# Optimization experiments

Measured on AMD Instinct MI355X. Metric: run time of the kernel, lower is better.

## Reference

```python
import jax, jax.numpy as jnp
import numpy as np

W_SIZE = 16
WIN = 2 * W_SIZE + 1
OUT_F = 256
MODEL = 512  # output_features * 2


def setup_inputs() -> dict:
    key = jax.random.key(0)
    ks = jax.random.split(key, 7)
    B, T = 4, 2048
    s = 0.02
    return {
        "x": jax.random.normal(ks[0], (B, T, MODEL), jnp.float32),
        "encoder_outputs": jax.random.normal(ks[1], (B, T, OUT_F), jnp.float32),
        # Attention: attn Linear (OUT_F + MODEL -> OUT_F), v Linear (OUT_F -> 1, no bias)
        "W_attn": jax.random.normal(ks[2], (OUT_F + MODEL, OUT_F), jnp.float32) * s,
        "b_attn": jnp.zeros((OUT_F,), jnp.float32),
        "v": jax.random.normal(ks[3], (OUT_F,), jnp.float32) * s,
        # final linear: (MODEL + OUT_F -> OUT_F)
        "W_lin": jax.random.normal(ks[4], (MODEL + OUT_F, OUT_F), jnp.float32) * s,
        "b_lin": jnp.zeros((OUT_F,), jnp.float32),
    }


def _windows(enc):
    B, T, F = enc.shape
    padded = jnp.pad(enc, ((0, 0), (W_SIZE, W_SIZE), (0, 0)))
    idx = jnp.arange(T)[:, None] + jnp.arange(WIN)[None, :]
    return padded[:, idx]


def reference(x, encoder_outputs, W_attn, b_attn, v, W_lin, b_lin):
    win = _windows(encoder_outputs)
    B, T, W, F = win.shape
    # additive (Bahdanau) score: concat(hidden, window) -> Linear -> tanh -> v
    Wh, We = W_attn[:MODEL], W_attn[MODEL:]
    energy = jnp.tanh(
        jnp.einsum('btm,mo->bto', x, Wh)[:, :, None, :]
        + jnp.einsum('btwf,fo->btwo', win, We)
        + b_attn
    )
    scores = jnp.einsum('btwo,o->btw', energy, v)
    a = jax.nn.softmax(scores, axis=-1)
    weighted = jnp.einsum('btw,btwf->btf', a, win)        # [B, T, F]
    h = jnp.concatenate([x, weighted], axis=-1)           # [B, T, MODEL+F]
    out = jax.nn.sigmoid(jnp.einsum('btk,ko->bto', h, W_lin) + b_lin)
    return out, a[:, :, None, :]
```

## Files before the change

### kernel.cpp

```cpp
#include <hip/hip_runtime.h>
#include <math.h>

#define T_DIM 2048
#define B_DIM 4
#define BT (B_DIM * T_DIM)
#define MODEL 512
#define OUTF 256
#define WSZ 16
#define WIN 33

#define BM 128
#define BN 64
#define BK 32

#define TB 16
#define HALO 48
#define TS 72

#define ESCALE 2.885390081777927f
#define ECLAMP 30.0f

typedef __attribute__((ext_vector_type(8))) short bf16x8;
typedef __attribute__((ext_vector_type(4))) float f32x4;

__device__ inline unsigned short f2bf(float f) {
  unsigned int u = __float_as_uint(f);
  u += 0x7fffu + ((u >> 16) & 1u);
  return (unsigned short)(u >> 16);
}
__device__ inline float bflo(unsigned int u) {
  return __uint_as_float(u << 16);
}
__device__ inline float bfhi(unsigned int u) {
  return __uint_as_float(u & 0xffff0000u);
}
__device__ inline float fast_sigmoid(float z) {
  return __builtin_amdgcn_rcpf(1.f + __expf(-z));
}

template <int KS, int MODE>
__device__ __forceinline__ void gemm_body(
    unsigned short (*As)[BM * 40], unsigned short (*Bs)[BN * 40], int rb,
    const float* __restrict__ A, int lda,
    const float* __restrict__ W_attn, const float* __restrict__ W_lin,
    const float* __restrict__ b_attn, const float* __restrict__ b_lin,
    unsigned short* __restrict__ outb, float* __restrict__ outf,
    unsigned short* __restrict__ outb2) {
  const int tid = threadIdx.x;
  const int cb = rb >> 6, rp = rb & 63;
  const int row0 = rp * BM;
  const int colg = (cb & 3) * 64;
  const float* Wsrc = (cb < 4) ? W_attn : W_lin;
  constexpr int wrow0 = (MODE == 0) ? 0 : 512;

  const int arow = tid >> 2, akp = (tid & 3) * 8;
  const int brow = tid >> 4, bcp = (tid & 15) * 4;
  const int bkey = (bcp >> 3) & 3;
  const float* aptr = A + (size_t)(row0 + arow) * lda + akp;
  const float* bptr = Wsrc + (size_t)(wrow0 + brow) * OUTF + colg + bcp;

  float4 ra0[2], ra1[2], rbw[2];
  auto LOADS = [&](int sl, int ks) {
    const float* ap = aptr + ks * BK;
    ra0[sl] = *(const float4*)ap;
    ra1[sl] = *(const float4*)(ap + 4);
    rbw[sl] = *(const float4*)(bptr + (size_t)ks * BK * OUTF);
  };
  auto WRITE = [&](int sl, int buf) {
    unsigned short t[8] = {f2bf(ra0[sl].x), f2bf(ra0[sl].y), f2bf(ra0[sl].z),
                           f2bf(ra0[sl].w), f2bf(ra1[sl].x), f2bf(ra1[sl].y),
                           f2bf(ra1[sl].z), f2bf(ra1[sl].w)};
    *(uint4*)&As[buf][arow * 40 + akp] = *(const uint4*)t;
    const int bk = brow ^ (bkey << 3);
    Bs[buf][(bcp + 0) * 40 + bk] = f2bf(rbw[sl].x);
    Bs[buf][(bcp + 1) * 40 + bk] = f2bf(rbw[sl].y);
    Bs[buf][(bcp + 2) * 40 + bk] = f2bf(rbw[sl].z);
    Bs[buf][(bcp + 3) * 40 + bk] = f2bf(rbw[sl].w);
  };

  const int w = tid >> 6, lane = tid & 63;
  const int lr = lane & 15, kg = lane >> 4;
  const int rbase = (w & 3) * 32;
  const int cbase = (w >> 2) * 32;
  const int bc0 = cbase + lr, bc1 = cbase + 16 + lr;
  const int bo0 = bc0 * 40 + ((kg ^ ((bc0 >> 3) & 3)) << 3);
  const int bo1 = bc1 * 40 + ((kg ^ ((bc1 >> 3) & 3)) << 3);

  f32x4 acc[2][2] = {{{0.f, 0.f, 0.f, 0.f}, {0.f, 0.f, 0.f, 0.f}},
                     {{0.f, 0.f, 0.f, 0.f}, {0.f, 0.f, 0.f, 0.f}}};

  LOADS(0, 0);
  if (KS > 1) LOADS(1, 1);
  WRITE(0, 0);
  __syncthreads();

#pragma unroll
  for (int ks = 0; ks < KS; ++ks) {
    if (ks + 2 < KS) LOADS(ks & 1, ks + 2);
    const int bf = ks & 1;
    bf16x8 a0 = *(const bf16x8*)&As[bf][(rbase + lr) * 40 + kg * 8];
    bf16x8 a1 = *(const bf16x8*)&As[bf][(rbase + 16 + lr) * 40 + kg * 8];
    bf16x8 b0 = *(const bf16x8*)&Bs[bf][bo0];
    bf16x8 b1 = *(const bf16x8*)&Bs[bf][bo1];
    acc[0][0] = __builtin_amdgcn_mfma_f32_16x16x32_bf16(a0, b0, acc[0][0], 0, 0, 0);
    acc[0][1] = __builtin_amdgcn_mfma_f32_16x16x32_bf16(a0, b1, acc[0][1], 0, 0, 0);
    acc[1][0] = __builtin_amdgcn_mfma_f32_16x16x32_bf16(a1, b0, acc[1][0], 0, 0, 0);
    acc[1][1] = __builtin_amdgcn_mfma_f32_16x16x32_bf16(a1, b1, acc[1][1], 0, 0, 0);
    if (ks + 1 < KS) WRITE((ks + 1) & 1, (ks + 1) & 1);
    __syncthreads();
  }

#pragma unroll
  for (int m = 0; m < 2; ++m) {
#pragma unroll
    for (int f = 0; f < 2; ++f) {
      const int col = colg + cbase + f * 16 + lr;
#pragma unroll
      for (int r = 0; r < 4; ++r) {
        const int row = row0 + rbase + m * 16 + kg * 4 + r;
        float val = acc[m][f][r];
        if (MODE == 0) {
          if (cb < 4) {
            const float y = fminf((val + b_attn[col]) * ESCALE, ECLAMP);
            outb[(size_t)row * OUTF + col] = f2bf(__builtin_amdgcn_exp2f(y));
          } else {
            outf[(size_t)row * OUTF + col] = val + b_lin[col];
          }
        } else {
          if (cb < 4) {
            const float y = fminf(val * ESCALE, ECLAMP);
            outb[(size_t)row * OUTF + col] = f2bf(__builtin_amdgcn_exp2f(y));
          } else {
            outb2[(size_t)row * OUTF + col] = f2bf(val);
          }
        }
      }
    }
  }
}

__global__ __launch_bounds__(512) void gemmAB_kernel(
    const float* __restrict__ x, const float* __restrict__ enc,
    const float* __restrict__ W_attn, const float* __restrict__ W_lin,
    const float* __restrict__ b_attn, const float* __restrict__ b_lin,
    unsigned short* __restrict__ xwe2, float* __restrict__ z1,
    unsigned short* __restrict__ ewe2, unsigned short* __restrict__ encWl2) {
  __shared__ unsigned short As[2][BM * 40];
  __shared__ unsigned short Bs[2][BN * 40];
  if (blockIdx.x < 512)
    gemm_body<16, 0>(As, Bs, blockIdx.x, x, MODEL, W_attn, W_lin, b_attn,
                     b_lin, xwe2, z1, nullptr);
  else
    gemm_body<8, 1>(As, Bs, blockIdx.x - 512, enc, OUTF, W_attn, W_lin,
                    nullptr, nullptr, ewe2, nullptr, encWl2);
}

__global__ __launch_bounds__(512) void attn_gemmc_kernel(
    const unsigned short* __restrict__ xwe2,
    const unsigned short* __restrict__ ewe2,
    const unsigned short* __restrict__ encWl2, const float* __restrict__ v,
    const float* __restrict__ z1, float* __restrict__ out,
    float* __restrict__ a_out) {
  __shared__ unsigned short EwT[256 * TS];
  __shared__ unsigned short Ab[TB * TS];

  const int tid = threadIdx.x;
  const int wv = tid >> 6, lane = tid & 63;
  const int rb = ((blockIdx.x & 7) << 6) | (blockIdx.x >> 3);
  const int t0 = rb * TB;
  const int b = t0 >> 11;
  const int tloc = t0 & (T_DIM - 1);
  const int g = lane >> 4, sl = lane & 15;

  if (tid < TB * TS / 8) ((uint4*)Ab)[tid] = make_uint4(0, 0, 0, 0);
  {
    const int col = tid >> 1, off = 48 + (tid & 1) * 8;
    const int kswz = ((col >> 3) & 7) << 3;
    *(uint4*)&EwT[col * TS + (off ^ kswz)] = make_uint4(0, 0, 0, 0);
  }

  for (int u = tid; u < HALO * 32; u += 512) {
    const int r = u >> 5, s = u & 31;
    const int tg = tloc - WSZ + r;
    uint4 qw = make_uint4(0, 0, 0, 0);
    if ((unsigned)tg < T_DIM)
      qw = *(const uint4*)(encWl2 + (((size_t)(b * T_DIM + tg)) << 8) + s * 8);
    unsigned short tt[8];
    *(uint4*)tt = qw;
    const int rsw = r ^ ((s & 7) << 3);
#pragma unroll
    for (int j = 0; j < 8; ++j) EwT[(s * 8 + j) * TS + rsw] = tt[j];
  }

  float vf[16];
  {
    const float4* vp = (const float4*)(v + sl * 16);
#pragma unroll
    for (int j = 0; j < 4; ++j) {
      float4 t4 = vp[j];
      vf[4 * j] = t4.x; vf[4 * j + 1] = t4.y;
      vf[4 * j + 2] = t4.z; vf[4 * j + 3] = t4.w;
    }
  }
  __syncthreads();

  const int lrow = wv * 2;
  const int bt0 = t0 + lrow, bt1 = bt0 + 1;

  float xe0[16], xe1[16];
  {
    const uint4* xp0 = (const uint4*)(xwe2 + ((size_t)bt0 << 8) + sl * 16);
    const uint4* xp1 = (const uint4*)(xwe2 + ((size_t)bt1 << 8) + sl * 16);
    uint4 q0 = xp0[0], q1 = xp0[1], q2 = xp1[0], q3 = xp1[1];
    unsigned int u0[8] = {q0.x, q0.y, q0.z, q0.w, q1.x, q1.y, q1.z, q1.w};
    unsigned int u1[8] = {q2.x, q2.y, q2.z, q2.w, q3.x, q3.y, q3.z, q3.w};
#pragma unroll
    for (int j = 0; j < 8; ++j) {
      xe0[2 * j] = bflo(u0[j]); xe0[2 * j + 1] = bfhi(u0[j]);
      xe1[2 * j] = bflo(u1[j]); xe1[2 * j + 1] = bfhi(u1[j]);
    }
  }

  const size_t bbase = ((size_t)(b * T_DIM)) << 8;
  const int tb0 = tloc + lrow - WSZ;
  float s0 = 0.f, s1 = 0.f;
#pragma unroll
  for (int c = 0; c < 9; ++c) {
    const int w_ = c * 4 + g;
    const int tg0 = tb0 + w_, tg1 = tg0 + 1;
    const bool vr0 = ((unsigned)tg0 < T_DIM);
    const bool vr1 = ((unsigned)tg1 < T_DIM);
    const uint4* p0 =
        (const uint4*)(ewe2 + bbase + (((size_t)(vr0 ? tg0 : 0)) << 8) + sl * 16);
    const uint4* p1 =
        (const uint4*)(ewe2 + bbase + (((size_t)(vr1 ? tg1 : 0)) << 8) + sl * 16);
    uint4 a0q = p0[0], a1q = p0[1];
    uint4 b0q = p1[0], b1q = p1[1];
    const uint4 ones =
        make_uint4(0x3f803f80u, 0x3f803f80u, 0x3f803f80u, 0x3f803f80u);
    if (!vr0) { a0q = ones; a1q = ones; }
    if (!vr1) { b0q = ones; b1q = ones; }
    unsigned int e0[8] = {a0q.x, a0q.y, a0q.z, a0q.w, a1q.x, a1q.y, a1q.z, a1q.w};
    unsigned int e1[8] = {b0q.x, b0q.y, b0q.z, b0q.w, b1q.x, b1q.y, b1q.z, b1q.w};
    float acc0 = 0.f, acc1 = 0.f;
#pragma unroll
    for (int j = 0; j < 8; ++j) {
      const float v0 = vf[2 * j], v1 = vf[2 * j + 1];
      const float vsj = v0 + v1;
      {
        const float E0 = xe0[2 * j] * bflo(e0[j]);
        const float E1 = xe0[2 * j + 1] * bfhi(e0[j]);
        const float den = (E0 + 1.f) * (E1 + 1.f);
        float num = fmaf(v0, E1, vsj);
        num = fmaf(v1, E0, num);
        acc0 = fmaf(num, __builtin_amdgcn_rcpf(den), acc0);
      }
      {
        const float E0 = xe1[2 * j] * bflo(e1[j]);
        const float E1 = xe1[2 * j + 1] * bfhi(e1[j]);
        const float den = (E0 + 1.f) * (E1 + 1.f);
        float num = fmaf(v0, E1, vsj);
        num = fmaf(v1, E0, num);
        acc1 = fmaf(num, __builtin_amdgcn_rcpf(den), acc1);
      }
    }
#pragma unroll
    for (int off = 1; off < 16; off <<= 1) {
      acc0 += __shfl_xor(acc0, off);
      acc1 += __shfl_xor(acc1, off);
    }
    const int src = (lane & 3) << 4;
    float c0v = __shfl(acc0, src), c1v = __shfl(acc1, src);
    if ((lane >> 2) == c) { s0 = c0v; s1 = c1v; }
  }

  float p0 = (lane < WIN) ? __builtin_amdgcn_exp2f(-ESCALE * s0) : 0.f;
  float p1 = (lane < WIN) ? __builtin_amdgcn_exp2f(-ESCALE * s1) : 0.f;
  float q0 = p0, q1 = p1;
#pragma unroll
  for (int off = 1; off < 64; off <<= 1) {
    q0 += __shfl_xor(q0, off);
    q1 += __shfl_xor(q1, off);
  }
  const float a0v = p0 * __builtin_amdgcn_rcpf(q0);
  const float a1v = p1 * __builtin_amdgcn_rcpf(q1);
  if (lane < WIN) {
    a_out[(size_t)bt0 * WIN + lane] = a0v;
    a_out[(size_t)bt1 * WIN + lane] = a1v;
    Ab[lrow * TS + lrow + lane] = f2bf(a0v);
    Ab[(lrow + 1) * TS + (lrow + 1) + lane] = f2bf(a1v);
  }
  __syncthreads();

  const int lr = lane & 15, kg = lane >> 4;
  f32x4 acc[2] = {{0.f, 0.f, 0.f, 0.f}, {0.f, 0.f, 0.f, 0.f}};
#pragma unroll
  for (int ks = 0; ks < 2; ++ks) {
    bf16x8 a = *(const bf16x8*)&Ab[lr * TS + ks * 32 + kg * 8];
#pragma unroll
    for (int f = 0; f < 2; ++f) {
      const int colB = wv * 32 + f * 16 + lr;
      const int kswz = ((colB >> 3) & 7) << 3;
      bf16x8 bb = *(const bf16x8*)&EwT[colB * TS + ((ks * 32 + kg * 8) ^ kswz)];
      acc[f] = __builtin_amdgcn_mfma_f32_16x16x32_bf16(a, bb, acc[f], 0, 0, 0);
    }
  }
#pragma unroll
  for (int f = 0; f < 2; ++f) {
    const int col = wv * 32 + f * 16 + lr;
#pragma unroll
    for (int r = 0; r < 4; ++r) {
      const int row = t0 + kg * 4 + r;
      out[(size_t)row * OUTF + col] =
          fast_sigmoid(acc[f][r] + z1[(size_t)row * OUTF + col]);
    }
  }
}

extern "C" void kernel_launch(void* const* d_in, const int* in_sizes, int n_in,
                              void* d_out, int out_size, void* d_ws,
                              size_t ws_size, hipStream_t stream) {
  const float* x      = (const float*)d_in[0];
  const float* enc    = (const float*)d_in[1];
  const float* W_attn = (const float*)d_in[2];
  const float* b_attn = (const float*)d_in[3];
  const float* v      = (const float*)d_in[4];
  const float* W_lin  = (const float*)d_in[5];
  const float* b_lin  = (const float*)d_in[6];

  float* out   = (float*)d_out;
  float* a_out = out + (size_t)BT * OUTF;

  unsigned short* xwe2   = (unsigned short*)d_ws;
  unsigned short* ewe2   = xwe2 + (size_t)BT * OUTF;
  unsigned short* encWl2 = ewe2 + (size_t)BT * OUTF;
  float*          z1     = (float*)(encWl2 + (size_t)BT * OUTF);

  gemmAB_kernel<<<1024, 512, 0, stream>>>(x, enc, W_attn, W_lin, b_attn,
                                          b_lin, xwe2, z1, ewe2, encWl2);
  attn_gemmc_kernel<<<512, 512, 0, stream>>>(xwe2, ewe2, encWl2, v, z1,
                                             out, a_out);
}
```

Before: 42.94 us.

## Widen GEMM tile to 128 columns and store z1 intermediate as bf16

The first GEMM kernel's tile grows from 128x64 to 128x128, so each wave computes a 32x64 sub-tile with four B fragments per k-step. This halves the block count and the redundant reloads of the A rows across column blocks. Separately, the x·W_lin partial result z1 is now written and read back as bf16 instead of fp32, halving that intermediate's memory traffic. This costs some precision in the final linear input, and the larger tile adds register pressure and leaves fewer blocks to fill the GPU.

```diff
diff --git a/kernel.cpp b/kernel.cpp
--- a/kernel.cpp
+++ b/kernel.cpp
@@ -10,7 +10,7 @@
 #define WIN 33
 
 #define BM 128
-#define BN 64
+#define BN 128
 #define BK 32
 
 #define TB 16
@@ -33,6 +33,9 @@
 }
 __device__ inline float bfhi(unsigned int u) {
   return __uint_as_float(u & 0xffff0000u);
+}
+__device__ inline float bfs(unsigned short u) {
+  return __uint_as_float(((unsigned int)u) << 16);
 }
 __device__ inline float fast_sigmoid(float z) {
   return __builtin_amdgcn_rcpf(1.f + __expf(-z));
@@ -44,27 +47,28 @@
     const float* __restrict__ A, int lda,
     const float* __restrict__ W_attn, const float* __restrict__ W_lin,
     const float* __restrict__ b_attn, const float* __restrict__ b_lin,
-    unsigned short* __restrict__ outb, float* __restrict__ outf,
-    unsigned short* __restrict__ outb2) {
+    unsigned short* __restrict__ outb, unsigned short* __restrict__ outb2) {
   const int tid = threadIdx.x;
-  const int cb = rb >> 6, rp = rb & 63;
+  const int cbg = rb >> 6, rp = rb & 63;
   const int row0 = rp * BM;
-  const int colg = (cb & 3) * 64;
-  const float* Wsrc = (cb < 4) ? W_attn : W_lin;
+  const float* Wsrc = (cbg < 2) ? W_attn : W_lin;
+  const int colw = (cbg & 1) * 128;
   constexpr int wrow0 = (MODE == 0) ? 0 : 512;
 
   const int arow = tid >> 2, akp = (tid & 3) * 8;
-  const int brow = tid >> 4, bcp = (tid & 15) * 4;
+  const int brow = tid >> 4, bcp = (tid & 15) * 8;
   const int bkey = (bcp >> 3) & 3;
   const float* aptr = A + (size_t)(row0 + arow) * lda + akp;
-  const float* bptr = Wsrc + (size_t)(wrow0 + brow) * OUTF + colg + bcp;
-
-  float4 ra0[2], ra1[2], rbw[2];
+  const float* bptr = Wsrc + (size_t)(wrow0 + brow) * OUTF + colw + bcp;
+
+  float4 ra0[2], ra1[2], rb0[2], rb1[2];
   auto LOADS = [&](int sl, int ks) {
     const float* ap = aptr + ks * BK;
     ra0[sl] = *(const float4*)ap;
     ra1[sl] = *(const float4*)(ap + 4);
-    rbw[sl] = *(const float4*)(bptr + (size_t)ks * BK * OUTF);
+    const float* bp = bptr + (size_t)ks * BK * OUTF;
+    rb0[sl] = *(const float4*)bp;
+    rb1[sl] = *(const float4*)(bp + 4);
   };
   auto WRITE = [&](int sl, int buf) {
     unsigned short t[8] = {f2bf(ra0[sl].x), f2bf(ra0[sl].y), f2bf(ra0[sl].z),
@@ -72,22 +76,32 @@
                            f2bf(ra1[sl].z), f2bf(ra1[sl].w)};
     *(uint4*)&As[buf][arow * 40 + akp] = *(const uint4*)t;
     const int bk = brow ^ (bkey << 3);
-    Bs[buf][(bcp + 0) * 40 + bk] = f2bf(rbw[sl].x);
-    Bs[buf][(bcp + 1) * 40 + bk] = f2bf(rbw[sl].y);
-    Bs[buf][(bcp + 2) * 40 + bk] = f2bf(rbw[sl].z);
-    Bs[buf][(bcp + 3) * 40 + bk] = f2bf(rbw[sl].w);
+    Bs[buf][(bcp + 0) * 40 + bk] = f2bf(rb0[sl].x);
+    Bs[buf][(bcp + 1) * 40 + bk] = f2bf(rb0[sl].y);
+    Bs[buf][(bcp + 2) * 40 + bk] = f2bf(rb0[sl].z);
+    Bs[buf][(bcp + 3) * 40 + bk] = f2bf(rb0[sl].w);
+    Bs[buf][(bcp + 4) * 40 + bk] = f2bf(rb1[sl].x);
+    Bs[buf][(bcp + 5) * 40 + bk] = f2bf(rb1[sl].y);
+    Bs[buf][(bcp + 6) * 40 + bk] = f2bf(rb1[sl].z);
+    Bs[buf][(bcp + 7) * 40 + bk] = f2bf(rb1[sl].w);
   };
 
   const int w = tid >> 6, lane = tid & 63;
   const int lr = lane & 15, kg = lane >> 4;
   const int rbase = (w & 3) * 32;
-  const int cbase = (w >> 2) * 32;
-  const int bc0 = cbase + lr, bc1 = cbase + 16 + lr;
-  const int bo0 = bc0 * 40 + ((kg ^ ((bc0 >> 3) & 3)) << 3);
-  const int bo1 = bc1 * 40 + ((kg ^ ((bc1 >> 3) & 3)) << 3);
-
-  f32x4 acc[2][2] = {{{0.f, 0.f, 0.f, 0.f}, {0.f, 0.f, 0.f, 0.f}},
-                     {{0.f, 0.f, 0.f, 0.f}, {0.f, 0.f, 0.f, 0.f}}};
+  const int cbase = (w >> 2) * 64;
+  int bo[4];
+#pragma unroll
+  for (int f = 0; f < 4; ++f) {
+    const int bc = cbase + f * 16 + lr;
+    bo[f] = bc * 40 + ((kg ^ ((bc >> 3) & 3)) << 3);
+  }
+
+  f32x4 acc[2][4];
+#pragma unroll
+  for (int m = 0; m < 2; ++m)
+#pragma unroll
+    for (int f = 0; f < 4; ++f) acc[m][f] = {0.f, 0.f, 0.f, 0.f};
 
   LOADS(0, 0);
   if (KS > 1) LOADS(1, 1);
@@ -100,12 +114,12 @@
     const int bf = ks & 1;
     bf16x8 a0 = *(const bf16x8*)&As[bf][(rbase + lr) * 40 + kg * 8];
     bf16x8 a1 = *(const bf16x8*)&As[bf][(rbase + 16 + lr) * 40 + kg * 8];
-    bf16x8 b0 = *(const bf16x8*)&Bs[bf][bo0];
-    bf16x8 b1 = *(const bf16x8*)&Bs[bf][bo1];
-    acc[0][0] = __builtin_amdgcn_mfma_f32_16x16x32_bf16(a0, b0, acc[0][0], 0, 0, 0);
-    acc[0][1] = __builtin_amdgcn_mfma_f32_16x16x32_bf16(a0, b1, acc[0][1], 0, 0, 0);
-    acc[1][0] = __builtin_amdgcn_mfma_f32_16x16x32_bf16(a1, b0, acc[1][0], 0, 0, 0);
-    acc[1][1] = __builtin_amdgcn_mfma_f32_16x16x32_bf16(a1, b1, acc[1][1], 0, 0, 0);
+#pragma unroll
+    for (int f = 0; f < 4; ++f) {
+      bf16x8 bb = *(const bf16x8*)&Bs[bf][bo[f]];
+      acc[0][f] = __builtin_amdgcn_mfma_f32_16x16x32_bf16(a0, bb, acc[0][f], 0, 0, 0);
+      acc[1][f] = __builtin_amdgcn_mfma_f32_16x16x32_bf16(a1, bb, acc[1][f], 0, 0, 0);
+    }
     if (ks + 1 < KS) WRITE((ks + 1) & 1, (ks + 1) & 1);
     __syncthreads();
   }
@@ -113,21 +127,21 @@
 #pragma unroll
   for (int m = 0; m < 2; ++m) {
 #pragma unroll
-    for (int f = 0; f < 2; ++f) {
-      const int col = colg + cbase + f * 16 + lr;
+    for (int f = 0; f < 4; ++f) {
+      const int col = (cbg & 1) * 128 + cbase + f * 16 + lr;
 #pragma unroll
       for (int r = 0; r < 4; ++r) {
         const int row = row0 + rbase + m * 16 + kg * 4 + r;
-        float val = acc[m][f][r];
+        const float val = acc[m][f][r];
         if (MODE == 0) {
-          if (cb < 4) {
+          if (cbg < 2) {
             const float y = fminf((val + b_attn[col]) * ESCALE, ECLAMP);
             outb[(size_t)row * OUTF + col] = f2bf(__builtin_amdgcn_exp2f(y));
           } else {
-            outf[(size_t)row * OUTF + col] = val + b_lin[col];
+            outb2[(size_t)row * OUTF + col] = f2bf(val + b_lin[col]);
           }
         } else {
-          if (cb < 4) {
+          if (cbg < 2) {
             const float y = fminf(val * ESCALE, ECLAMP);
             outb[(size_t)row * OUTF + col] = f2bf(__builtin_amdgcn_exp2f(y));
           } else {
@@ -143,23 +157,23 @@
     const float* __restrict__ x, const float* __restrict__ enc,
     const float* __restrict__ W_attn, const float* __restrict__ W_lin,
     const float* __restrict__ b_attn, const float* __restrict__ b_lin,
-    unsigned short* __restrict__ xwe2, float* __restrict__ z1,
+    unsigned short* __restrict__ xwe2, unsigned short* __restrict__ z1b,
     unsigned short* __restrict__ ewe2, unsigned short* __restrict__ encWl2) {
   __shared__ unsigned short As[2][BM * 40];
   __shared__ unsigned short Bs[2][BN * 40];
-  if (blockIdx.x < 512)
+  if (blockIdx.x < 256)
     gemm_body<16, 0>(As, Bs, blockIdx.x, x, MODEL, W_attn, W_lin, b_attn,
-                     b_lin, xwe2, z1, nullptr);
+                     b_lin, xwe2, z1b);
   else
-    gemm_body<8, 1>(As, Bs, blockIdx.x - 512, enc, OUTF, W_attn, W_lin,
-                    nullptr, nullptr, ewe2, nullptr, encWl2);
+    gemm_body<8, 1>(As, Bs, blockIdx.x - 256, enc, OUTF, W_attn, W_lin,
+                    nullptr, nullptr, ewe2, encWl2);
 }
 
 __global__ __launch_bounds__(512) void attn_gemmc_kernel(
     const unsigned short* __restrict__ xwe2,
     const unsigned short* __restrict__ ewe2,
     const unsigned short* __restrict__ encWl2, const float* __restrict__ v,
-    const float* __restrict__ z1, float* __restrict__ out,
+    const unsigned short* __restrict__ z1b, float* __restrict__ out,
     float* __restrict__ a_out) {
   __shared__ unsigned short EwT[256 * TS];
   __shared__ unsigned short Ab[TB * TS];
@@ -311,8 +325,8 @@
 #pragma unroll
     for (int r = 0; r < 4; ++r) {
       const int row = t0 + kg * 4 + r;
-      out[(size_t)row * OUTF + col] =
-          fast_sigmoid(acc[f][r] + z1[(size_t)row * OUTF + col]);
+      out[(size_t)row * OUTF + col] = fast_sigmoid(
+          acc[f][r] + bfs(z1b[(size_t)row * OUTF + col]));
     }
   }
 }
@@ -334,10 +348,10 @@
   unsigned short* xwe2   = (unsigned short*)d_ws;
   unsigned short* ewe2   = xwe2 + (size_t)BT * OUTF;
   unsigned short* encWl2 = ewe2 + (size_t)BT * OUTF;
-  float*          z1     = (float*)(encWl2 + (size_t)BT * OUTF);
-
-  gemmAB_kernel<<<1024, 512, 0, stream>>>(x, enc, W_attn, W_lin, b_attn,
-                                          b_lin, xwe2, z1, ewe2, encWl2);
-  attn_gemmc_kernel<<<512, 512, 0, stream>>>(xwe2, ewe2, encWl2, v, z1,
+  unsigned short* z1b    = encWl2 + (size_t)BT * OUTF;
+
+  gemmAB_kernel<<<512, 512, 0, stream>>>(x, enc, W_attn, W_lin, b_attn,
+                                         b_lin, xwe2, z1b, ewe2, encWl2);
+  attn_gemmc_kernel<<<512, 512, 0, stream>>>(xwe2, ewe2, encWl2, v, z1b,
                                              out, a_out);
 }
```

Result: no change. 43.73 us (+1.8%).
